# Performance work log

Measured on AMD Instinct MI355X. Metric: run time of the kernel, lower is better.

Reference implementation:

```python
import jax, jax.numpy as jnp
import numpy as np

M = 2048      # mention groups (spans with antecedents)
K_MAX = 128   # max antecedents per mention
N = 4096      # candidate span pool
G = 1000      # span representation dim
D = 20        # distance/genre/speaker embed dim
H = 150       # Score MLP hidden
GIJ = 3 * G + 3 * D  # 3060


def setup_inputs() -> dict:
    key = jax.random.key(0)
    ks = jax.random.split(key, 12)
    # ragged group lengths (deterministic): cycle 1..K_MAX, sum = P = 132096
    lengths = np.tile(np.arange(1, K_MAX + 1), M // K_MAX).astype(np.int32)
    P = int(lengths.sum())
    seg_ids = np.repeat(np.arange(M), lengths).astype(np.int32)
    starts = np.cumsum(lengths) - lengths
    offsets = (np.arange(P) - starts[seg_ids]).astype(np.int32)

    genre_emb = jax.random.normal(ks[3], (8, D), jnp.float32) * 0.02
    genre_emb = genre_emb.at[0].set(0.0)   # padding_idx=0
    speaker_emb = jax.random.normal(ks[4], (3, D), jnp.float32) * 0.02
    speaker_emb = speaker_emb.at[0].set(0.0)  # padding_idx=0

    return {
        "g_i": jax.random.normal(ks[0], (N, G), jnp.float32),
        "mention_scores": jax.random.normal(ks[1], (N, 1), jnp.float32),
        "dist_emb": jax.random.normal(ks[2], (9, D), jnp.float32) * 0.02,
        "genre_emb": genre_emb,
        "speaker_emb": speaker_emb,
        "W1": jax.random.normal(ks[5], (GIJ, H), jnp.float32) / np.sqrt(GIJ),
        "b1": jnp.zeros((H,), jnp.float32),
        "W2": jax.random.normal(ks[6], (H, H), jnp.float32) / np.sqrt(H),
        "b2": jnp.zeros((H,), jnp.float32),
        "W3": jax.random.normal(ks[7], (H, 1), jnp.float32) / np.sqrt(H),
        "b3": jnp.zeros((1,), jnp.float32),
        "mention_ids": jax.random.randint(ks[8], (P,), 0, N, jnp.int32),
        "antecedent_ids": jax.random.randint(ks[9], (P,), 0, N, jnp.int32),
        "dist_ids": jax.random.randint(ks[10], (P,), 0, 9, jnp.int32),
        "genre_ids": jax.random.randint(ks[11], (P,), 0, 8, jnp.int32),
        "speaker_ids": jax.random.randint(jax.random.fold_in(key, 99), (P,), 0, 3, jnp.int32),
        "lengths": jnp.asarray(lengths),
        "seg_ids": jnp.asarray(seg_ids),
        "offsets": jnp.asarray(offsets),
    }


def reference(g_i, mention_scores, dist_emb, genre_emb, speaker_emb,
              W1, b1, W2, b2, W3, b3,
              mention_ids, antecedent_ids, dist_ids, genre_ids, speaker_ids,
              lengths, seg_ids, offsets):
    # feature gathers: phi = [distance, genre, speaker] embeddings, (P, 3D)
    phi = jnp.concatenate(
        [dist_emb[dist_ids], genre_emb[genre_ids], speaker_emb[speaker_ids]], axis=1)
    i_g = g_i[mention_ids]      # (P, G)
    j_g = g_i[antecedent_ids]   # (P, G)
    pairs = jnp.concatenate([i_g, j_g, i_g * j_g, phi], axis=1)  # (P, GIJ)

    # 3-layer scoring MLP (dropout inactive at eval)
    h = jax.nn.relu(pairs @ W1 + b1)
    h = jax.nn.relu(h @ W2 + b2)
    s_ij = (h @ W3 + b3)[:, 0]  # (P,)

    scores = mention_scores[mention_ids, 0] + mention_scores[antecedent_ids, 0] + s_ij

    # per-group softmax over [group scores, epsilon=0] via segment ops
    seg_max = jax.ops.segment_max(scores, seg_ids, num_segments=M)
    m = jnp.maximum(seg_max, 0.0)                      # include epsilon 0
    e = jnp.exp(scores - m[seg_ids])                   # (P,)
    eps_e = jnp.exp(-m)                                # (M,)
    denom = jax.ops.segment_sum(e, seg_ids, num_segments=M) + eps_e
    pair_probs = e / denom[seg_ids]                    # (P,)
    eps_probs = eps_e / denom                          # (M,)

    # pad_and_stack(value=1000): row 0 is the empty leading group -> [1, 1000...]
    grid = jnp.full((M + 1, K_MAX + 1), 1000.0, dtype=scores.dtype)
    grid = grid.at[seg_ids + 1, offsets].set(pair_probs)
    grid = grid.at[jnp.arange(M) + 1, lengths].set(eps_probs)
    grid = grid.at[0, 0].set(1.0)
    return grid
```

## Files before the change

kernel.cpp:

```cpp
#include <hip/hip_runtime.h>

#define P_TOTAL 132096
#define NPOOL   4096
#define GDIM    1000
#define HDIM    150
#define MGRP    2048
#define KMAX    128

typedef __attribute__((ext_vector_type(4))) float f32x4;
typedef __attribute__((ext_vector_type(2))) float f32x2;
typedef __attribute__((ext_vector_type(4))) unsigned int u32x4;

#define OFF_W1C8   0
#define OFF_W1AB8  163840
#define OFF_W2F8   491520
#define OFF_ABPRE  517120
#define OFF_TABS2  3138560
#define OFF_SGRID  3276800
#define OFF_GF8    4325376
#define OFF_EXTRAS 8519680

__device__ __forceinline__ short f2bf(float f) {
  union { float f; unsigned u; } v; v.f = f;
  unsigned r = v.u + 0x7FFFu + ((v.u >> 16) & 1u);
  return (short)(r >> 16);
}
__device__ __forceinline__ float bf2f(unsigned short s) {
  return __builtin_bit_cast(float, ((unsigned)s) << 16);
}
__device__ __forceinline__ unsigned char f2fp8(float f) {
  int d = __builtin_amdgcn_cvt_pk_fp8_f32(f, 0.f, 0, false);
  return (unsigned char)(d & 0xFF);
}
__device__ __forceinline__ long mk64(unsigned lo, unsigned hi) {
  return (long)(((unsigned long long)hi << 32) | lo);
}

__device__ __forceinline__ u32x4 fp8prod16(u32x4 m, u32x4 a) {
  u32x4 r;
  #pragma unroll
  for (int d = 0; d < 4; ++d) {
    f32x2 ml = __builtin_amdgcn_cvt_pk_f32_fp8(m[d], false);
    f32x2 mh = __builtin_amdgcn_cvt_pk_f32_fp8(m[d], true);
    f32x2 al = __builtin_amdgcn_cvt_pk_f32_fp8(a[d], false);
    f32x2 ah = __builtin_amdgcn_cvt_pk_f32_fp8(a[d], true);
    f32x2 pl = ml * al, ph = mh * ah;
    int o = __builtin_amdgcn_cvt_pk_fp8_f32(pl[0], pl[1], 0, false);
    o = __builtin_amdgcn_cvt_pk_fp8_f32(ph[0], ph[1], o, true);
    r[d] = (unsigned)o;
  }
  return r;
}

#define S1 5120
#define S2 10240
#define S3 800
#define S4 (NPOOL*256)
#define S5 (216*160)
__global__ __launch_bounds__(256) void prep_kernel(
    const float* __restrict__ W1, const float* __restrict__ W2,
    const float* __restrict__ g_i,
    const float* __restrict__ dist_emb, const float* __restrict__ genre_emb,
    const float* __restrict__ spk_emb, const float* __restrict__ b1,
    unsigned char* __restrict__ w1c8, unsigned char* __restrict__ w1ab8,
    unsigned char* __restrict__ w2f8, unsigned* __restrict__ gf8,
    float* __restrict__ tabs2) {
  int idx = blockIdx.x * 256 + threadIdx.x;
  if (idx < S1) {
    int c = idx / 160, n = idx % 160;
    int s = c >> 1, j = c & 1;
    unsigned dw[8];
    #pragma unroll
    for (int d = 0; d < 8; ++d) {
      unsigned acc = 0;
      #pragma unroll
      for (int b = 0; b < 4; ++b) {
        int kk = d*4 + b;
        int g = kk >> 3, i = kk & 7;
        int q = g ^ ((n >> 2) & 3);
        int k = s*64 + q*16 + j*8 + i;
        float v = (k < GDIM && n < HDIM) ? W1[(2000 + k)*HDIM + n] : 0.f;
        acc |= ((unsigned)f2fp8(v)) << (8*b);
      }
      dw[d] = acc;
    }
    u32x4 lo = {dw[0], dw[1], dw[2], dw[3]};
    u32x4 hi = {dw[4], dw[5], dw[6], dw[7]};
    *(u32x4*)(w1c8 + c*5120 + n*32)      = lo;
    *(u32x4*)(w1c8 + c*5120 + n*32 + 16) = hi;
  } else if (idx < S1 + S2) {
    int i2 = idx - S1;
    int c = i2 / 320, n = i2 % 320;
    int s = c >> 2, j = c & 3;
    unsigned dw[8];
    #pragma unroll
    for (int d = 0; d < 8; ++d) {
      unsigned acc = 0;
      #pragma unroll
      for (int b = 0; b < 4; ++b) {
        int kk = d*4 + b;
        int g = kk >> 3, i = kk & 7;
        int k = s*128 + g*32 + j*8 + i;
        float v = 0.f;
        if (k < GDIM) {
          if (n < HDIM)                 v = W1[k*HDIM + n];
          else if (n >= 160 && n < 310) v = W1[(1000 + k)*HDIM + (n - 160)];
        }
        acc |= ((unsigned)f2fp8(v)) << (8*b);
      }
      dw[d] = acc;
    }
    u32x4 lo = {dw[0], dw[1], dw[2], dw[3]};
    u32x4 hi = {dw[4], dw[5], dw[6], dw[7]};
    *(u32x4*)(w1ab8 + c*10240 + n*32)      = lo;
    *(u32x4*)(w1ab8 + c*10240 + n*32 + 16) = hi;
  } else if (idx < S1 + S2 + S3) {
    int i2 = idx - S1 - S2;
    int c = i2 / 160, n = i2 % 160;
    unsigned dw[8];
    #pragma unroll
    for (int d = 0; d < 8; ++d) {
      unsigned acc = 0;
      #pragma unroll
      for (int b = 0; b < 4; ++b) {
        int kk = d*4 + b;
        int g = kk >> 3, ii = kk & 7;
        int q = g ^ ((n >> 2) & 3);
        int k = c*32 + q*8 + ii;
        float v = (k < HDIM && n < HDIM) ? W2[k*HDIM + n] : 0.f;
        acc |= ((unsigned)f2fp8(v)) << (8*b);
      }
      dw[d] = acc;
    }
    u32x4 lo = {dw[0], dw[1], dw[2], dw[3]};
    u32x4 hi = {dw[4], dw[5], dw[6], dw[7]};
    *(u32x4*)(w2f8 + c*5120 + n*32)      = lo;
    *(u32x4*)(w2f8 + c*5120 + n*32 + 16) = hi;
  } else if (idx < S1 + S2 + S3 + S4) {
    int i = idx - S1 - S2 - S3;
    int row = i >> 8, jd = i & 255;
    int c0 = jd * 4;
    float f0 = (c0     < GDIM) ? g_i[row*GDIM + c0]     : 0.f;
    float f1 = (c0 + 1 < GDIM) ? g_i[row*GDIM + c0 + 1] : 0.f;
    float f2 = (c0 + 2 < GDIM) ? g_i[row*GDIM + c0 + 2] : 0.f;
    float f3 = (c0 + 3 < GDIM) ? g_i[row*GDIM + c0 + 3] : 0.f;
    int d = 0;
    d = __builtin_amdgcn_cvt_pk_fp8_f32(f0, f1, d, false);
    d = __builtin_amdgcn_cvt_pk_fp8_f32(f2, f3, d, true);
    gf8[i] = (unsigned)d;
  } else if (idx < S1 + S2 + S3 + S4 + S5) {
    int i = idx - S1 - S2 - S3 - S4;
    int row = i / 160, n = i % 160;
    float acc = 0.f;
    if (n < HDIM) {
      int d = row / 24, g = (row / 3) % 8, sp = row % 3;
      acc = b1[n];
      #pragma unroll
      for (int kk = 0; kk < 20; ++kk) {
        acc += dist_emb [d*20 + kk]  * W1[(3000 + kk)*HDIM + n];
        acc += genre_emb[g*20 + kk]  * W1[(3020 + kk)*HDIM + n];
        acc += spk_emb  [sp*20 + kk] * W1[(3040 + kk)*HDIM + n];
      }
    }
    tabs2[i] = acc;
  }
}

__global__ __launch_bounds__(128) void pre_gemm_kernel(
    const unsigned char* __restrict__ gf8, const unsigned char* __restrict__ w1ab8,
    unsigned short* __restrict__ abpre) {
  int wave = threadIdx.x >> 6, lane = threadIdx.x & 63;
  int quad = lane >> 4, n16 = lane & 15;
  int rowbase = blockIdx.x * 32 + wave * 16;
  int colbase = blockIdx.y * 80;

  f32x4 acc[5];
  #pragma unroll
  for (int t = 0; t < 5; ++t) acc[t] = (f32x4){0.f, 0.f, 0.f, 0.f};

  const unsigned char* arow = gf8 + (long)(rowbase + n16) * 1024 + quad*32;

  for (int s = 0; s < 8; ++s) {
    u32x4 Aa = *(const u32x4*)(arow + s*128);
    u32x4 Ab = *(const u32x4*)(arow + s*128 + 16);
    #pragma unroll
    for (int j = 0; j < 4; ++j) {
      long a = (j == 0) ? mk64(Aa[0], Aa[1]) : (j == 1) ? mk64(Aa[2], Aa[3])
             : (j == 2) ? mk64(Ab[0], Ab[1]) : mk64(Ab[2], Ab[3]);
      const unsigned char* bp = w1ab8 + (((s*4 + j)*320 + colbase + n16) * 32 + quad*8);
      #pragma unroll
      for (int t = 0; t < 5; ++t) {
        long b = *(const long*)(bp + t*16*32);
        acc[t] = __builtin_amdgcn_mfma_f32_16x16x32_fp8_fp8(a, b, acc[t], 0, 0, 0);
      }
    }
  }
  #pragma unroll
  for (int t = 0; t < 5; ++t) {
    #pragma unroll
    for (int r = 0; r < 4; ++r) {
      int row = rowbase + quad*4 + r;
      abpre[(long)row * 320 + colbase + t*16 + n16] = (unsigned short)f2bf(acc[t][r]);
    }
  }
}

__global__ __launch_bounds__(256) void extras_kernel(
    const unsigned* __restrict__ abpre32, const float* __restrict__ tabs2,
    const int* __restrict__ mid, const int* __restrict__ aid,
    const int* __restrict__ did, const int* __restrict__ gid,
    const int* __restrict__ sid,
    unsigned* __restrict__ extras32, int pbase) {
  int t = threadIdx.x;
  int lp = blockIdx.x * 16 + (t >> 4);
  int p = pbase + lp;
  int l = t & 15;
  int m = mid[p], a = aid[p];
  int itab = did[p]*24 + gid[p]*3 + sid[p];
  const unsigned* pm = abpre32 + (long)m*160;
  const unsigned* pa = abpre32 + (long)a*160 + 80;
  const f32x2* tb = (const f32x2*)(tabs2 + (long)itab*160);
  #pragma unroll
  for (int j = 0; j < 5; ++j) {
    int d = l + j*16;
    unsigned um = pm[d], ua = pa[d];
    f32x2 tt = tb[d];
    float v0 = bf2f((unsigned short)(um & 0xffff)) + bf2f((unsigned short)(ua & 0xffff)) + tt[0];
    float v1 = bf2f((unsigned short)(um >> 16))    + bf2f((unsigned short)(ua >> 16))    + tt[1];
    unsigned o = ((unsigned)(unsigned short)f2bf(v0))
               | (((unsigned)(unsigned short)f2bf(v1)) << 16);
    extras32[(long)lp*80 + d] = o;
  }
}

__global__ __launch_bounds__(256) void mlp_kernel(
    const unsigned char* __restrict__ gf8,
    const unsigned short* __restrict__ extras,
    const unsigned char* __restrict__ w1c8,
    const unsigned char* __restrict__ w2f8,
    const float* __restrict__ ms,
    const float* __restrict__ W3, const float* __restrict__ b2,
    const float* __restrict__ b3,
    const int* __restrict__ mention_ids, const int* __restrict__ antecedent_ids,
    const int* __restrict__ seg_ids, const int* __restrict__ offs,
    float* __restrict__ sgrid, int pbase) {

  __shared__ __align__(16) unsigned char lds[53248];

  int tid = threadIdx.x;
  int wave = tid >> 6, lane = tid & 63;
  int quad = lane >> 4, n16 = lane & 15;
  int lp0 = blockIdx.x * 128;
  int gp0 = pbase + lp0;
  int wrow = wave * 32;

  int jj = (lane & 3) ^ ((lane >> 2) & 3) ^ ((lane >> 4) & 1);
  int srow = lane >> 2;
  int swA = quad ^ (n16 & 3) ^ ((n16 >> 2) & 1);
  int swB = quad ^ ((n16 >> 2) & 3);

  const unsigned char* pA0 =
      gf8 + (long)mention_ids[gp0 + wave*16 + srow] * 1024 + jj*16;
  const unsigned char* pA1 =
      gf8 + (long)mention_ids[gp0 + (wave + 4)*16 + srow] * 1024 + jj*16;
  const unsigned char* pA2 =
      gf8 + (long)antecedent_ids[gp0 + wave*16 + srow] * 1024 + jj*16;
  const unsigned char* pA3 =
      gf8 + (long)antecedent_ids[gp0 + (wave + 4)*16 + srow] * 1024 + jj*16;
  int dA0 = wave*1024,      dA1 = (wave + 4)*1024;
  int dA2 = 8192 + dA0,     dA3 = 8192 + dA1;

  f32x4 acc0[10], acc1[10];
  #pragma unroll
  for (int t = 0; t < 10; ++t) {
    acc0[t] = (f32x4){0.f, 0.f, 0.f, 0.f};
    acc1[t] = (f32x4){0.f, 0.f, 0.f, 0.f};
  }

  auto issue = [&](int s, int buf) {
    unsigned char* base = lds + buf*26624;
    long so = (long)s * 64;
    __builtin_amdgcn_global_load_lds((const unsigned int*)(pA0 + so),
        (unsigned int*)(base + dA0 + lane*16), 16, 0, 0);
    __builtin_amdgcn_global_load_lds((const unsigned int*)(pA1 + so),
        (unsigned int*)(base + dA1 + lane*16), 16, 0, 0);
    __builtin_amdgcn_global_load_lds((const unsigned int*)(pA2 + so),
        (unsigned int*)(base + dA2 + lane*16), 16, 0, 0);
    __builtin_amdgcn_global_load_lds((const unsigned int*)(pA3 + so),
        (unsigned int*)(base + dA3 + lane*16), 16, 0, 0);
    const unsigned char* wsrc = w1c8 + (long)s*10240;
    __builtin_amdgcn_global_load_lds((const unsigned int*)(wsrc + wave*1024 + (long)lane*16),
        (unsigned int*)(base + 16384 + wave*1024 + lane*16), 16, 0, 0);
    __builtin_amdgcn_global_load_lds((const unsigned int*)(wsrc + (wave+4)*1024 + (long)lane*16),
        (unsigned int*)(base + 16384 + (wave+4)*1024 + lane*16), 16, 0, 0);
    if (wave < 2)
      __builtin_amdgcn_global_load_lds((const unsigned int*)(wsrc + (wave+8)*1024 + (long)lane*16),
          (unsigned int*)(base + 16384 + (wave+8)*1024 + lane*16), 16, 0, 0);
  };

  issue(0, 0);
  for (int s = 0; s < 16; ++s) {
    __syncthreads();
    if (s < 15) issue(s + 1, (s + 1) & 1);
    const unsigned char* cb = lds + (s & 1)*26624;

    u32x4 M0 = *(const u32x4*)(cb + (wrow + n16)*64 + swA*16);
    u32x4 C0 = *(const u32x4*)(cb + 8192 + (wrow + n16)*64 + swA*16);
    u32x4 M1 = *(const u32x4*)(cb + (wrow + 16 + n16)*64 + swA*16);
    u32x4 C1 = *(const u32x4*)(cb + 8192 + (wrow + 16 + n16)*64 + swA*16);
    u32x4 P0 = fp8prod16(M0, C0);
    u32x4 P1 = fp8prod16(M1, C1);

    #pragma unroll
    for (int j = 0; j < 2; ++j) {
      long a0 = (j == 0) ? mk64(P0[0], P0[1]) : mk64(P0[2], P0[3]);
      long a1 = (j == 0) ? mk64(P1[0], P1[1]) : mk64(P1[2], P1[3]);
      const unsigned char* bp = cb + 16384 + j*5120 + n16*32 + swB*8;
      #pragma unroll
      for (int t = 0; t < 10; ++t) {
        long b = *(const long*)(bp + t*512);
        acc0[t] = __builtin_amdgcn_mfma_f32_16x16x32_fp8_fp8(a0, b, acc0[t], 0, 0, 0);
        acc1[t] = __builtin_amdgcn_mfma_f32_16x16x32_fp8_fp8(a1, b, acc1[t], 0, 0, 0);
      }
    }
  }
  __syncthreads();

  for (int r = wave; r < 25; r += 4) {
    __builtin_amdgcn_global_load_lds(
        (const unsigned int*)(w2f8 + r*1024 + (long)lane*16),
        (unsigned int*)(lds + 26624 + r*1024), 16, 0, 0);
  }

  unsigned char* h1w = lds + wave * 5888;
  #pragma unroll
  for (int t = 0; t < 10; ++t) {
    int n = t*16 + n16;
    #pragma unroll
    for (int r = 0; r < 4; ++r) {
      int row0 = quad*4 + r;
      float v0 = acc0[t][r] + bf2f(extras[(long)(lp0 + wrow + row0)*160 + n]);
      float v1 = acc1[t][r] + bf2f(extras[(long)(lp0 + wrow + 16 + row0)*160 + n]);
      h1w[row0*184 + n]        = f2fp8(fmaxf(v0, 0.f));
      h1w[(16 + row0)*184 + n] = f2fp8(fmaxf(v1, 0.f));
    }
  }
  __syncthreads();

  float bias3 = b3[0];
  float w3v[10], b2v[10];
  #pragma unroll
  for (int t = 0; t < 10; ++t) {
    int n = t*16 + n16;
    w3v[t] = (n < HDIM) ? W3[n] : 0.f;
    b2v[t] = (n < HDIM) ? b2[n] : 0.f;
  }

  #pragma unroll
  for (int tile = 0; tile < 2; ++tile) {
    f32x4 acc2[10];
    #pragma unroll
    for (int t = 0; t < 10; ++t) acc2[t] = (f32x4){0.f, 0.f, 0.f, 0.f};

    #pragma unroll
    for (int c = 0; c < 5; ++c) {
      long a = *(const long*)(h1w + (tile*16 + n16)*184 + c*32 + quad*8);
      const unsigned char* bp = lds + 26624 + (c*160 + n16)*32 + swB*8;
      #pragma unroll
      for (int t = 0; t < 10; ++t) {
        long b = *(const long*)(bp + t*512);
        acc2[t] = __builtin_amdgcn_mfma_f32_16x16x32_fp8_fp8(a, b, acc2[t], 0, 0, 0);
      }
    }

    float part[4] = {0.f, 0.f, 0.f, 0.f};
    #pragma unroll
    for (int t = 0; t < 10; ++t) {
      #pragma unroll
      for (int r = 0; r < 4; ++r) {
        float h2 = fmaxf(acc2[t][r] + b2v[t], 0.f);
        part[r] += h2 * w3v[t];
      }
    }
    for (int msk = 1; msk < 16; msk <<= 1) {
      #pragma unroll
      for (int r = 0; r < 4; ++r) part[r] += __shfl_xor(part[r], msk);
    }

    if (n16 == 0) {
      #pragma unroll
      for (int r = 0; r < 4; ++r) {
        int gp = gp0 + wrow + tile*16 + quad*4 + r;
        float sc = part[r] + bias3 + ms[mention_ids[gp]] + ms[antecedent_ids[gp]];
        sgrid[seg_ids[gp] * KMAX + offs[gp]] = sc;
      }
    }
  }
}

__global__ __launch_bounds__(128) void softmax_kernel(const float* __restrict__ sgrid,
                                                      const int* __restrict__ lengths,
                                                      float* __restrict__ out) {
  int b = blockIdx.x, t = threadIdx.x;
  if (b == 0) {
    out[t] = (t == 0) ? 1.0f : 1000.0f;
    if (t == 0) out[128] = 1000.0f;
    return;
  }
  int m = b - 1;
  int len = lengths[m];
  float s = (t < len) ? sgrid[m * KMAX + t] : -1e30f;

  __shared__ float redA[2];
  __shared__ float redB[2];

  float v = s;
  #pragma unroll
  for (int o = 32; o >= 1; o >>= 1) v = fmaxf(v, __shfl_xor(v, o));
  if ((t & 63) == 0) redA[t >> 6] = v;
  __syncthreads();
  float mx = fmaxf(fmaxf(redA[0], redA[1]), 0.0f);

  float e = (t < len) ? expf(s - mx) : 0.f;
  float sum = e;
  #pragma unroll
  for (int o = 32; o >= 1; o >>= 1) sum += __shfl_xor(sum, o);
  if ((t & 63) == 0) redB[t >> 6] = sum;
  __syncthreads();

  float eps_e = expf(-mx);
  float denom = redB[0] + redB[1] + eps_e;

  float* row = out + (long)(m + 1) * 129;
  float val;
  if (t < len)       val = e / denom;
  else if (t == len) val = eps_e / denom;
  else               val = 1000.0f;
  row[t] = val;
  if (t == 0) row[128] = (len == KMAX) ? (eps_e / denom) : 1000.0f;
}

extern "C" void kernel_launch(void* const* d_in, const int* in_sizes, int n_in,
                              void* d_out, int out_size, void* d_ws, size_t ws_size,
                              hipStream_t stream) {
  const float* g_i        = (const float*)d_in[0];
  const float* ms         = (const float*)d_in[1];
  const float* dist_emb   = (const float*)d_in[2];
  const float* genre_emb  = (const float*)d_in[3];
  const float* spk_emb    = (const float*)d_in[4];
  const float* W1         = (const float*)d_in[5];
  const float* b1         = (const float*)d_in[6];
  const float* W2         = (const float*)d_in[7];
  const float* b2         = (const float*)d_in[8];
  const float* W3         = (const float*)d_in[9];
  const float* b3         = (const float*)d_in[10];
  const int* mention_ids    = (const int*)d_in[11];
  const int* antecedent_ids = (const int*)d_in[12];
  const int* dist_ids       = (const int*)d_in[13];
  const int* genre_ids      = (const int*)d_in[14];
  const int* spk_ids        = (const int*)d_in[15];
  const int* lengths        = (const int*)d_in[16];
  const int* seg_ids        = (const int*)d_in[17];
  const int* offsets        = (const int*)d_in[18];

  char* ws = (char*)d_ws;
  unsigned char* w1c8  = (unsigned char*)(ws + OFF_W1C8);
  unsigned char* w1ab8 = (unsigned char*)(ws + OFF_W1AB8);
  unsigned char* w2f8  = (unsigned char*)(ws + OFF_W2F8);
  unsigned short* abpre = (unsigned short*)(ws + OFF_ABPRE);
  float* tabs2  = (float*)(ws + OFF_TABS2);
  float* sgrid  = (float*)(ws + OFF_SGRID);
  unsigned char* gf8  = (unsigned char*)(ws + OFF_GF8);
  unsigned short* extras = (unsigned short*)(ws + OFF_EXTRAS);

  size_t avail = (ws_size > OFF_EXTRAS) ? ws_size - OFF_EXTRAS : 0;
  int nchunk;
  if      (avail >= (size_t)P_TOTAL * 320)      nchunk = 1;
  else if (avail >= (size_t)P_TOTAL * 160)      nchunk = 2;
  else if (avail >= (size_t)P_TOTAL * 80)       nchunk = 4;
  else                                          nchunk = 8;
  int npc = P_TOTAL / nchunk;

  const int prepN = S1 + S2 + S3 + S4 + S5;
  prep_kernel<<<(prepN + 255)/256, 256, 0, stream>>>(W1, W2, g_i,
                                                     dist_emb, genre_emb, spk_emb, b1,
                                                     w1c8, w1ab8, w2f8,
                                                     (unsigned*)gf8, tabs2);
  dim3 gpre(NPOOL/32, 4);
  pre_gemm_kernel<<<gpre, 128, 0, stream>>>(gf8, w1ab8, abpre);
  for (int c = 0; c < nchunk; ++c) {
    int pbase = c * npc;
    extras_kernel<<<npc/16, 256, 0, stream>>>((const unsigned*)abpre, tabs2,
                                              mention_ids, antecedent_ids,
                                              dist_ids, genre_ids, spk_ids,
                                              (unsigned*)extras, pbase);
    mlp_kernel<<<npc/128, 256, 0, stream>>>(gf8, extras, w1c8, w2f8, ms,
                                            W3, b2, b3,
                                            mention_ids, antecedent_ids,
                                            seg_ids, offsets, sgrid, pbase);
  }
  softmax_kernel<<<MGRP + 1, 128, 0, stream>>>(sgrid, lengths, (float*)d_out);
}
```

Baseline: 206.9 us.

## Triple-buffer layer-1 LDS pipeline with explicit vmcnt waits and MFMA priority

Replaces the double-buffered layer-1 loop with a three-stage LDS ring, issuing loads two stages ahead. It uses explicit s_waitcnt vmcnt counts and raw s_barrier calls instead of __syncthreads, so loads stay in flight across barriers. It also raises wave priority around the MFMA block. The W2 and h1 staging regions are moved so the larger 78 KB LDS allocation is reused. The cost is more LDS per block, which may lower occupancy, and the hardcoded vmcnt values must match the number of loads each issue() call makes.

```diff
diff --git a/kernel.cpp b/kernel.cpp
--- a/kernel.cpp
+++ b/kernel.cpp
@@ -50,6 +50,12 @@
     r[d] = (unsigned)o;
   }
   return r;
+}
+
+__device__ __forceinline__ void barrier_f() {
+  asm volatile("" ::: "memory");
+  __builtin_amdgcn_s_barrier();
+  asm volatile("" ::: "memory");
 }
 
 #define S1 5120
@@ -245,7 +251,7 @@
     const int* __restrict__ seg_ids, const int* __restrict__ offs,
     float* __restrict__ sgrid, int pbase) {
 
-  __shared__ __align__(16) unsigned char lds[53248];
+  __shared__ __align__(16) unsigned char lds[79872];
 
   int tid = threadIdx.x;
   int wave = tid >> 6, lane = tid & 63;
@@ -298,12 +304,8 @@
           (unsigned int*)(base + 16384 + (wave+8)*1024 + lane*16), 16, 0, 0);
   };
 
-  issue(0, 0);
-  for (int s = 0; s < 16; ++s) {
-    __syncthreads();
-    if (s < 15) issue(s + 1, (s + 1) & 1);
-    const unsigned char* cb = lds + (s & 1)*26624;
-
+  auto compute = [&](int buf) {
+    const unsigned char* cb = lds + buf*26624;
     u32x4 M0 = *(const u32x4*)(cb + (wrow + n16)*64 + swA*16);
     u32x4 C0 = *(const u32x4*)(cb + 8192 + (wrow + n16)*64 + swA*16);
     u32x4 M1 = *(const u32x4*)(cb + (wrow + 16 + n16)*64 + swA*16);
@@ -311,6 +313,7 @@
     u32x4 P0 = fp8prod16(M0, C0);
     u32x4 P1 = fp8prod16(M1, C1);
 
+    __builtin_amdgcn_s_setprio(1);
     #pragma unroll
     for (int j = 0; j < 2; ++j) {
       long a0 = (j == 0) ? mk64(P0[0], P0[1]) : mk64(P0[2], P0[3]);
@@ -323,16 +326,36 @@
         acc1[t] = __builtin_amdgcn_mfma_f32_16x16x32_fp8_fp8(a1, b, acc1[t], 0, 0, 0);
       }
     }
-  }
+    __builtin_amdgcn_s_setprio(0);
+  };
+
+  issue(0, 0);
+  issue(1, 1);
+  int bi = 2, ci = 0;
+  for (int s = 0; s < 14; ++s) {
+    issue(s + 2, bi);
+    asm volatile("s_waitcnt vmcnt(12)" ::: "memory");
+    barrier_f();
+    compute(ci);
+    barrier_f();
+    bi = ci;
+    ci = (ci == 2) ? 0 : ci + 1;
+  }
+  asm volatile("s_waitcnt vmcnt(6)" ::: "memory");
+  barrier_f();
+  compute(2);
+  asm volatile("s_waitcnt vmcnt(0)" ::: "memory");
+  barrier_f();
+  compute(0);
   __syncthreads();
 
   for (int r = wave; r < 25; r += 4) {
     __builtin_amdgcn_global_load_lds(
         (const unsigned int*)(w2f8 + r*1024 + (long)lane*16),
-        (unsigned int*)(lds + 26624 + r*1024), 16, 0, 0);
-  }
-
-  unsigned char* h1w = lds + wave * 5888;
+        (unsigned int*)(lds + r*1024), 16, 0, 0);
+  }
+
+  unsigned char* h1w = lds + 26624 + wave * 5888;
   #pragma unroll
   for (int t = 0; t < 10; ++t) {
     int n = t*16 + n16;
@@ -365,7 +388,7 @@
     #pragma unroll
     for (int c = 0; c < 5; ++c) {
       long a = *(const long*)(h1w + (tile*16 + n16)*184 + c*32 + quad*8);
-      const unsigned char* bp = lds + 26624 + (c*160 + n16)*32 + swB*8;
+      const unsigned char* bp = lds + (c*160 + n16)*32 + swB*8;
       #pragma unroll
       for (int t = 0; t < 10; ++t) {
         long b = *(const long*)(bp + t*512);
```

Result: slower. 211.1 us (+2.0%).

## Fuse extras gather into MLP epilogue and drop materialized extras buffer

Applied to the files above, without the earlier changes.

Removes the separate extras kernel that wrote a per-pair bf16 buffer of layer-1 partial sums (about 42 MB) and then read it back in the MLP kernel. The MLP epilogue now gathers the precomputed mention/antecedent partials from abpre and the feature-table row directly, using a byte-sized table index computed in the prep kernel. This avoids the large write-plus-read round trip, the extra launches and the chunking logic. In exchange the MLP epilogue does scattered gathers with more dependent loads per row, and the sum is no longer rounded through bf16.

```diff
diff --git a/kernel.cpp b/kernel.cpp
--- a/kernel.cpp
+++ b/kernel.cpp
@@ -18,7 +18,7 @@
 #define OFF_TABS2  3138560
 #define OFF_SGRID  3276800
 #define OFF_GF8    4325376
-#define OFF_EXTRAS 8519680
+#define OFF_ITAB   8519680
 
 __device__ __forceinline__ short f2bf(float f) {
   union { float f; unsigned u; } v; v.f = f;
@@ -57,14 +57,17 @@
 #define S3 800
 #define S4 (NPOOL*256)
 #define S5 (216*160)
+#define S6 P_TOTAL
 __global__ __launch_bounds__(256) void prep_kernel(
     const float* __restrict__ W1, const float* __restrict__ W2,
     const float* __restrict__ g_i,
     const float* __restrict__ dist_emb, const float* __restrict__ genre_emb,
     const float* __restrict__ spk_emb, const float* __restrict__ b1,
+    const int* __restrict__ did, const int* __restrict__ gid,
+    const int* __restrict__ sid,
     unsigned char* __restrict__ w1c8, unsigned char* __restrict__ w1ab8,
     unsigned char* __restrict__ w2f8, unsigned* __restrict__ gf8,
-    float* __restrict__ tabs2) {
+    float* __restrict__ tabs2, unsigned char* __restrict__ itab8) {
   int idx = blockIdx.x * 256 + threadIdx.x;
   if (idx < S1) {
     int c = idx / 160, n = idx % 160;
@@ -163,6 +166,9 @@
       }
     }
     tabs2[i] = acc;
+  } else if (idx < S1 + S2 + S3 + S4 + S5 + S6) {
+    int p = idx - (S1 + S2 + S3 + S4 + S5);
+    itab8[p] = (unsigned char)(did[p]*24 + gid[p]*3 + sid[p]);
   }
 }
 
@@ -205,37 +211,11 @@
   }
 }
 
-__global__ __launch_bounds__(256) void extras_kernel(
-    const unsigned* __restrict__ abpre32, const float* __restrict__ tabs2,
-    const int* __restrict__ mid, const int* __restrict__ aid,
-    const int* __restrict__ did, const int* __restrict__ gid,
-    const int* __restrict__ sid,
-    unsigned* __restrict__ extras32, int pbase) {
-  int t = threadIdx.x;
-  int lp = blockIdx.x * 16 + (t >> 4);
-  int p = pbase + lp;
-  int l = t & 15;
-  int m = mid[p], a = aid[p];
-  int itab = did[p]*24 + gid[p]*3 + sid[p];
-  const unsigned* pm = abpre32 + (long)m*160;
-  const unsigned* pa = abpre32 + (long)a*160 + 80;
-  const f32x2* tb = (const f32x2*)(tabs2 + (long)itab*160);
-  #pragma unroll
-  for (int j = 0; j < 5; ++j) {
-    int d = l + j*16;
-    unsigned um = pm[d], ua = pa[d];
-    f32x2 tt = tb[d];
-    float v0 = bf2f((unsigned short)(um & 0xffff)) + bf2f((unsigned short)(ua & 0xffff)) + tt[0];
-    float v1 = bf2f((unsigned short)(um >> 16))    + bf2f((unsigned short)(ua >> 16))    + tt[1];
-    unsigned o = ((unsigned)(unsigned short)f2bf(v0))
-               | (((unsigned)(unsigned short)f2bf(v1)) << 16);
-    extras32[(long)lp*80 + d] = o;
-  }
-}
-
 __global__ __launch_bounds__(256) void mlp_kernel(
     const unsigned char* __restrict__ gf8,
-    const unsigned short* __restrict__ extras,
+    const unsigned short* __restrict__ abpre,
+    const float* __restrict__ tabs2,
+    const unsigned char* __restrict__ itab8,
     const unsigned char* __restrict__ w1c8,
     const unsigned char* __restrict__ w2f8,
     const float* __restrict__ ms,
@@ -243,7 +223,7 @@
     const float* __restrict__ b3,
     const int* __restrict__ mention_ids, const int* __restrict__ antecedent_ids,
     const int* __restrict__ seg_ids, const int* __restrict__ offs,
-    float* __restrict__ sgrid, int pbase) {
+    float* __restrict__ sgrid) {
 
   __shared__ __align__(16) unsigned char lds[53248];
 
@@ -251,7 +231,7 @@
   int wave = tid >> 6, lane = tid & 63;
   int quad = lane >> 4, n16 = lane & 15;
   int lp0 = blockIdx.x * 128;
-  int gp0 = pbase + lp0;
+  int gp0 = lp0;
   int wrow = wave * 32;
 
   int jj = (lane & 3) ^ ((lane >> 2) & 3) ^ ((lane >> 4) & 1);
@@ -334,13 +314,21 @@
 
   unsigned char* h1w = lds + wave * 5888;
   #pragma unroll
-  for (int t = 0; t < 10; ++t) {
-    int n = t*16 + n16;
-    #pragma unroll
-    for (int r = 0; r < 4; ++r) {
-      int row0 = quad*4 + r;
-      float v0 = acc0[t][r] + bf2f(extras[(long)(lp0 + wrow + row0)*160 + n]);
-      float v1 = acc1[t][r] + bf2f(extras[(long)(lp0 + wrow + 16 + row0)*160 + n]);
+  for (int r = 0; r < 4; ++r) {
+    int row0 = quad*4 + r;
+    int gpA = gp0 + wrow + row0;
+    int gpB = gpA + 16;
+    const unsigned short* pmA = abpre + (long)mention_ids[gpA]*320;
+    const unsigned short* paA = abpre + (long)antecedent_ids[gpA]*320 + 160;
+    const float*          tbA = tabs2 + (long)itab8[gpA]*160;
+    const unsigned short* pmB = abpre + (long)mention_ids[gpB]*320;
+    const unsigned short* paB = abpre + (long)antecedent_ids[gpB]*320 + 160;
+    const float*          tbB = tabs2 + (long)itab8[gpB]*160;
+    #pragma unroll
+    for (int t = 0; t < 10; ++t) {
+      int n = t*16 + n16;
+      float v0 = acc0[t][r] + bf2f(pmA[n]) + bf2f(paA[n]) + tbA[n];
+      float v1 = acc1[t][r] + bf2f(pmB[n]) + bf2f(paB[n]) + tbB[n];
       h1w[row0*184 + n]        = f2fp8(fmaxf(v0, 0.f));
       h1w[(16 + row0)*184 + n] = f2fp8(fmaxf(v1, 0.f));
     }
@@ -471,33 +459,20 @@
   float* tabs2  = (float*)(ws + OFF_TABS2);
   float* sgrid  = (float*)(ws + OFF_SGRID);
   unsigned char* gf8  = (unsigned char*)(ws + OFF_GF8);
-  unsigned short* extras = (unsigned short*)(ws + OFF_EXTRAS);
-
-  size_t avail = (ws_size > OFF_EXTRAS) ? ws_size - OFF_EXTRAS : 0;
-  int nchunk;
-  if      (avail >= (size_t)P_TOTAL * 320)      nchunk = 1;
-  else if (avail >= (size_t)P_TOTAL * 160)      nchunk = 2;
-  else if (avail >= (size_t)P_TOTAL * 80)       nchunk = 4;
-  else                                          nchunk = 8;
-  int npc = P_TOTAL / nchunk;
-
-  const int prepN = S1 + S2 + S3 + S4 + S5;
+  unsigned char* itab8 = (unsigned char*)(ws + OFF_ITAB);
+
+  const int prepN = S1 + S2 + S3 + S4 + S5 + S6;
   prep_kernel<<<(prepN + 255)/256, 256, 0, stream>>>(W1, W2, g_i,
                                                      dist_emb, genre_emb, spk_emb, b1,
+                                                     dist_ids, genre_ids, spk_ids,
                                                      w1c8, w1ab8, w2f8,
-                                                     (unsigned*)gf8, tabs2);
+                                                     (unsigned*)gf8, tabs2, itab8);
   dim3 gpre(NPOOL/32, 4);
   pre_gemm_kernel<<<gpre, 128, 0, stream>>>(gf8, w1ab8, abpre);
-  for (int c = 0; c < nchunk; ++c) {
-    int pbase = c * npc;
-    extras_kernel<<<npc/16, 256, 0, stream>>>((const unsigned*)abpre, tabs2,
+  mlp_kernel<<<P_TOTAL/128, 256, 0, stream>>>(gf8, abpre, tabs2, itab8,
+                                              w1c8, w2f8, ms,
+                                              W3, b2, b3,
                                               mention_ids, antecedent_ids,
-                                              dist_ids, genre_ids, spk_ids,
-                                              (unsigned*)extras, pbase);
-    mlp_kernel<<<npc/128, 256, 0, stream>>>(gf8, extras, w1c8, w2f8, ms,
-                                            W3, b2, b3,
-                                            mention_ids, antecedent_ids,
-                                            seg_ids, offsets, sgrid, pbase);
-  }
+                                              seg_ids, offsets, sgrid);
   softmax_kernel<<<MGRP + 1, 128, 0, stream>>>(sgrid, lengths, (float*)d_out);
 }
```

New measurement: 199.7 us, median of 3. 1.04x faster.
